# Kernel optimization log

Measured on AMD Instinct MI355X. Metric: run time of the kernel, lower is better.

The kernel has to match this reference:

```python
import jax, jax.numpy as jnp
import numpy as np

# Longformer-base-4096 dims; attention_window=128 -> one-sided window 64
B, S, D, H, L, F, V, NUM_LABELS = 1, 4096, 768, 12, 12, 3072, 50265, 100
DH = D // H
W = 64            # one-sided sliding window
NC = S // W       # number of query chunks
EPS = 1e-5
SCALE = float(1.0 / np.sqrt(DH))


def layer_norm(x, s, b):
    m = jnp.mean(x, axis=-1, keepdims=True)
    v = jnp.mean(jnp.square(x - m), axis=-1, keepdims=True)
    return (x - m) * jax.lax.rsqrt(v + EPS) * s + b


def heads(x):  # [B,S,D] -> [B,H,S,DH]
    return x.reshape(B, S, H, DH).transpose(0, 2, 1, 3)


def chunk3(t):  # [B,H,S,DH] -> [B,H,NC,3W,DH]: key blocks c-1,c,c+1 per query chunk c
    tp = jnp.pad(t, ((0, 0), (0, 0), (W, W), (0, 0)))
    tb = tp.reshape(B, H, NC + 2, W, DH)
    return jnp.concatenate([tb[:, :, i:i + NC] for i in range(3)], axis=3)


def _forward(input_ids, attention_mask, emb_tok, emb_pos, ln_emb_scale, ln_emb_bias,
             Wq, bq, Wk, bk, Wv, bv, Wqg, bqg, Wkg, bkg, Wvg, bvg, Wo, bo,
             ln1_scale, ln1_bias, Wf1, bf1, Wf2, bf2, ln2_scale, ln2_bias, Wc, bc):
    am = attention_mask > 0                      # [B,S]
    x = layer_norm(emb_tok[input_ids] + emb_pos[None, :, :], ln_emb_scale, ln_emb_bias)

    # static sliding-window masks, shared by all layers
    qi = jnp.arange(W)[:, None]
    kj = jnp.arange(3 * W)[None, :]
    band = (kj >= qi) & (kj <= qi + 2 * W)       # |key - query| <= W within a chunk triple
    kvalid = am & (jnp.arange(S)[None, :] > 0)   # global token (pos 0) excluded from window
    kp = jnp.pad(kvalid, ((0, 0), (W, W))).reshape(B, NC + 2, W)
    kmask = jnp.concatenate([kp[:, i:i + NC] for i in range(3)], axis=2)   # [B,NC,3W]
    win_mask = band[None, None, None] & kmask[:, None, :, None, :]         # [B,1,NC,W,3W]

    def layer(x, p):
        (wq, bq_, wk, bk_, wv, bv_, wqg, bqg_, wkg, bkg_, wvg, bvg_, wo, bo_,
         l1s, l1b, wf1, bf1_, wf2, bf2_, l2s, l2b) = p
        q = heads(x @ wq + bq_) * SCALE
        k = heads(x @ wk + bk_)
        v = heads(x @ wv + bv_)
        qc = q.reshape(B, H, NC, W, DH)
        k3, v3 = chunk3(k), chunk3(v)
        sc = jnp.einsum('bhcqd,bhckd->bhcqk', qc, k3)          # [B,H,NC,W,3W]
        sc = jnp.where(win_mask, sc, -1e9)
        # every token also attends to the global CLS key (standard K/V of pos 0)
        sg = jnp.einsum('bhsd,bhd->bhs', q, k[:, :, 0]).reshape(B, H, NC, W, 1)
        probs = jax.nn.softmax(jnp.concatenate([sg, sc], axis=-1), axis=-1)
        pg, pl = probs[..., 0], probs[..., 1:]
        ctx = jnp.einsum('bhcqk,bhckd->bhcqd', pl, v3).reshape(B, H, S, DH)
        ctx = ctx + pg.reshape(B, H, S, 1) * v[:, :, :1]
        # global token attends to everything with its own (global) projections
        qg = heads(x @ wqg + bqg_)[:, :, 0] * SCALE            # [B,H,DH]
        kg = heads(x @ wkg + bkg_)
        vg = heads(x @ wvg + bvg_)
        sgl = jnp.where(am[:, None, :], jnp.einsum('bhd,bhjd->bhj', qg, kg), -1e9)
        ctx0 = jnp.einsum('bhj,bhjd->bhd', jax.nn.softmax(sgl, axis=-1), vg)
        ctx = ctx.at[:, :, 0].set(ctx0)
        attn = ctx.transpose(0, 2, 1, 3).reshape(B, S, D) @ wo + bo_
        x1 = layer_norm(x + attn, l1s, l1b)
        h = jax.nn.gelu(x1 @ wf1 + bf1_, approximate=False)
        return layer_norm(x1 + h @ wf2 + bf2_, l2s, l2b), None

    params = (Wq, bq, Wk, bk, Wv, bv, Wqg, bqg, Wkg, bkg, Wvg, bvg, Wo, bo,
              ln1_scale, ln1_bias, Wf1, bf1, Wf2, bf2, ln2_scale, ln2_bias)
    x, _ = jax.lax.scan(layer, x, params)
    return x[:, 0] @ Wc + bc                                   # [B, NUM_LABELS]


def setup_inputs():
    key = jax.random.key(0)
    ks = jax.random.split(key, 40)
    it = iter(range(40))
    nrm = lambda shape: jax.random.normal(ks[next(it)], shape, dtype=jnp.float32) * 0.02
    z = lambda shape: jnp.zeros(shape, jnp.float32)
    o = lambda shape: jnp.ones(shape, jnp.float32)
    return {
        'input_ids': jax.random.randint(ks[next(it)], (B, S), 0, V, dtype=jnp.int32),
        'attention_mask': jnp.ones((B, S), dtype=jnp.int32),
        'emb_tok': nrm((V, D)), 'emb_pos': nrm((S, D)),
        'ln_emb_scale': o((D,)), 'ln_emb_bias': z((D,)),
        'Wq': nrm((L, D, D)), 'bq': z((L, D)),
        'Wk': nrm((L, D, D)), 'bk': z((L, D)),
        'Wv': nrm((L, D, D)), 'bv': z((L, D)),
        'Wqg': nrm((L, D, D)), 'bqg': z((L, D)),
        'Wkg': nrm((L, D, D)), 'bkg': z((L, D)),
        'Wvg': nrm((L, D, D)), 'bvg': z((L, D)),
        'Wo': nrm((L, D, D)), 'bo': z((L, D)),
        'ln1_scale': o((L, D)), 'ln1_bias': z((L, D)),
        'Wf1': nrm((L, D, F)), 'bf1': z((L, F)),
        'Wf2': nrm((L, F, D)), 'bf2': z((L, D)),
        'ln2_scale': o((L, D)), 'ln2_bias': z((L, D)),
        'Wc': nrm((D, NUM_LABELS)), 'bc': z((NUM_LABELS,)),
    }


def reference(input_ids, attention_mask, emb_tok, emb_pos, ln_emb_scale, ln_emb_bias,
              Wq, bq, Wk, bk, Wv, bv, Wqg, bqg, Wkg, bkg, Wvg, bvg, Wo, bo,
              ln1_scale, ln1_bias, Wf1, bf1, Wf2, bf2, ln2_scale, ln2_bias, Wc, bc):
    return _forward(input_ids, attention_mask, emb_tok, emb_pos, ln_emb_scale, ln_emb_bias,
                    Wq, bq, Wk, bk, Wv, bv, Wqg, bqg, Wkg, bkg, Wvg, bvg, Wo, bo,
                    ln1_scale, ln1_bias, Wf1, bf1, Wf2, bf2, ln2_scale, ln2_bias, Wc, bc)
```

## Files before the change

### kernel.cpp

```cpp
#include <hip/hip_runtime.h>
#include <hip/hip_bf16.h>

typedef unsigned short u16;
typedef __attribute__((ext_vector_type(8))) short bf16x8;
typedef __attribute__((ext_vector_type(4))) float f32x4;

constexpr int S = 4096, D = 768, H = 12, NL = 12, F = 3072, NLAB = 100, DH = 64;
constexpr int NQKV = 3840;
constexpr float SCALE = 0.125f;
constexpr float EPS = 1e-5f;

__device__ __forceinline__ float bits2f(u16 u) {
  union { unsigned int i; float f; } x; x.i = ((unsigned int)u) << 16; return x.f;
}
__device__ __forceinline__ u16 f2bbits(float f) {
  union { float f; unsigned int i; } x; x.f = f;
  return (u16)((x.i + 0x7FFFu + ((x.i >> 16) & 1u)) >> 16);
}
__device__ __forceinline__ float rdw(const void* p, size_t i, int isf32) {
  return isf32 ? ((const float*)p)[i] : bits2f(((const u16*)p)[i]);
}
__device__ __forceinline__ void gload16(const void* g, void* l) {
  __builtin_amdgcn_global_load_lds(
      (const __attribute__((address_space(1))) void*)g,
      (__attribute__((address_space(3))) void*)l, 16, 0, 0);
}

__global__ void detect_k(const void* lns, int* flag) {
  *flag = (*(const unsigned int*)lns == 0x3F800000u) ? 1 : 0;
}

struct PrepArgs {
  const void *Wq, *Wk, *Wv, *Wkg, *Wvg, *Wo, *Wqg, *Wf1, *Wf2;
  const void *bq, *bk, *bv, *bkg, *bvg, *bo, *bqg, *bf1, *bf2;
  size_t oDD, oDF, oD, oF;
  u16 *wt_qkv, *wt_o, *wt_qg, *wt_f1, *wt_f2;
  float* biasb;
  const int* flag;
};

__global__ __launch_bounds__(256) void prep_layer(PrepArgs a)
{
  const int b = blockIdx.x, t = threadIdx.x;
  const int isf32 = *a.flag;
  if (b < 8640) {
    __shared__ float tile[32][33];
    const void* src; size_t soff; int N, ld, rowoff, n0, k0;
    u16* dst; float scl = 1.f;
    if (b < 4032) {
      const int m = b / 576, ti = b - m * 576;
      soff = a.oDD; N = D; ld = D; rowoff = 0;
      switch (m) {
        case 0:  src = a.Wq;  dst = a.wt_qkv; scl = SCALE;  break;
        case 1:  src = a.Wk;  dst = a.wt_qkv; rowoff = 768; break;
        case 2:  src = a.Wv;  dst = a.wt_qkv; rowoff = 1536; break;
        case 3:  src = a.Wkg; dst = a.wt_qkv; rowoff = 2304; break;
        case 4:  src = a.Wvg; dst = a.wt_qkv; rowoff = 3072; break;
        case 5:  src = a.Wo;  dst = a.wt_o;   break;
        default: src = a.Wqg; dst = a.wt_qg;  scl = SCALE;  break;
      }
      n0 = (ti % 24) * 32; k0 = (ti / 24) * 32;
    } else if (b < 6336) {
      const int ti = b - 4032;
      src = a.Wf1; soff = a.oDF; N = F; dst = a.wt_f1; rowoff = 0; ld = D;
      n0 = (ti % 96) * 32; k0 = (ti / 96) * 32;
    } else {
      const int ti = b - 6336;
      src = a.Wf2; soff = a.oDF; N = D; dst = a.wt_f2; rowoff = 0; ld = F;
      n0 = (ti % 24) * 32; k0 = (ti / 24) * 32;
    }
    const int r = t >> 3, cc = (t & 7) << 2;
    const size_t si = soff + (size_t)(k0 + r) * N + n0 + cc;
    if (isf32) {
      const float4 v = *reinterpret_cast<const float4*>(&((const float*)src)[si]);
      tile[r][cc] = v.x * scl; tile[r][cc+1] = v.y * scl;
      tile[r][cc+2] = v.z * scl; tile[r][cc+3] = v.w * scl;
    } else {
      const ushort4 v = *reinterpret_cast<const ushort4*>(&((const u16*)src)[si]);
      tile[r][cc] = bits2f(v.x) * scl; tile[r][cc+1] = bits2f(v.y) * scl;
      tile[r][cc+2] = bits2f(v.z) * scl; tile[r][cc+3] = bits2f(v.w) * scl;
    }
    __syncthreads();
    const ushort4 ov = make_ushort4(f2bbits(tile[cc+0][r]), f2bbits(tile[cc+1][r]),
                                    f2bbits(tile[cc+2][r]), f2bbits(tile[cc+3][r]));
    *reinterpret_cast<ushort4*>(&dst[(size_t)(rowoff + n0 + r) * ld + k0 + cc]) = ov;
  } else {
    const int i = (b - 8640) * 256 + t;
    float v;
    if      (i < 768)  v = rdw(a.bq,  a.oD + i,        isf32) * SCALE;
    else if (i < 1536) v = rdw(a.bk,  a.oD + i - 768,  isf32);
    else if (i < 2304) v = rdw(a.bv,  a.oD + i - 1536, isf32);
    else if (i < 3072) v = rdw(a.bkg, a.oD + i - 2304, isf32);
    else if (i < 3840) v = rdw(a.bvg, a.oD + i - 3072, isf32);
    else if (i < 4608) v = rdw(a.bo,  a.oD + i - 3840, isf32);
    else if (i < 7680) v = rdw(a.bf1, a.oF + i - 4608, isf32);
    else if (i < 8448) v = rdw(a.bf2, a.oD + i - 7680, isf32);
    else               v = rdw(a.bqg, a.oD + i - 8448, isf32) * SCALE;
    a.biasb[i] = v;
  }
}

template<int BN>
__global__ __launch_bounds__(256) void mfma_gemm(
    const u16* __restrict__ A, const u16* __restrict__ BT,
    const float* __restrict__ bias,
    float* __restrict__ Cf, u16* __restrict__ Cb,
    int M, int N, int K, int act)
{
  constexpr int BM = 128, BK = 32;
  constexpr int WN = BN / 2;
  constexpr int NR = WN / 16;
  __shared__ u16 As[BM * BK];
  __shared__ u16 Bs[BN * BK];
  const int t = threadIdx.x;
  const int wid = t >> 6, lane = t & 63;
  const int wr = wid >> 1, wc = wid & 1;
  const int m0 = blockIdx.y * BM, n0 = blockIdx.x * BN;
  const int l_row = lane >> 2;
  const int l_kc = (lane & 3) << 3;

  f32x4 acc[4][NR];
#pragma unroll
  for (int m = 0; m < 4; ++m)
#pragma unroll
    for (int n = 0; n < NR; ++n)
      acc[m][n] = (f32x4){0.f, 0.f, 0.f, 0.f};

  const int frow = lane & 15;
  const int fkb = (lane >> 4) << 3;

  for (int kt = 0; kt < K; kt += BK) {
#pragma unroll
    for (int i = 0; i < 2; ++i) {
      const int ch = wid * 2 + i;
      gload16(&A[(size_t)(m0 + ch * 16 + l_row) * K + kt + l_kc], &As[ch * 512]);
    }
#pragma unroll
    for (int i = 0; i < BN / 64; ++i) {
      const int ch = wid * (BN / 64) + i;
      gload16(&BT[(size_t)(n0 + ch * 16 + l_row) * K + kt + l_kc], &Bs[ch * 512]);
    }
    __syncthreads();
    bf16x8 af[4], bfr[NR];
#pragma unroll
    for (int m = 0; m < 4; ++m)
      af[m] = *reinterpret_cast<const bf16x8*>(&As[(wr * 64 + m * 16 + frow) * BK + fkb]);
#pragma unroll
    for (int n = 0; n < NR; ++n)
      bfr[n] = *reinterpret_cast<const bf16x8*>(&Bs[(wc * WN + n * 16 + frow) * BK + fkb]);
#pragma unroll
    for (int m = 0; m < 4; ++m)
#pragma unroll
      for (int n = 0; n < NR; ++n)
        acc[m][n] = __builtin_amdgcn_mfma_f32_16x16x32_bf16(af[m], bfr[n], acc[m][n], 0, 0, 0);
    __syncthreads();
  }

  const int crow = (lane >> 4) << 2;
  const int ccol = lane & 15;
#pragma unroll
  for (int m = 0; m < 4; ++m) {
#pragma unroll
    for (int n = 0; n < NR; ++n) {
      const int gc = n0 + wc * WN + n * 16 + ccol;
      const float bv = bias[gc];
#pragma unroll
      for (int r = 0; r < 4; ++r) {
        const int gr = m0 + wr * 64 + m * 16 + crow + r;
        float x = acc[m][n][r] + bv;
        if (act) x = 0.5f * x * (1.0f + erff(x * 0.70710678118654752f));
        if (Cf) Cf[(size_t)gr * N + gc] = x;
        if (Cb) Cb[(size_t)gr * N + gc] = f2bbits(x);
      }
    }
  }
}

__global__ void embed_k(const int* __restrict__ ids, const void* __restrict__ tok,
                        const void* __restrict__ pos, float* __restrict__ out,
                        const int* __restrict__ flag)
{
  const int isf32 = *flag;
  const int s = blockIdx.x, t = threadIdx.x;
  const int id = ids[s];
  for (int c = t; c < D; c += 256)
    out[(size_t)s * D + c] = rdw(tok, (size_t)id * D + c, isf32) + rdw(pos, (size_t)s * D + c, isf32);
}

__global__ __launch_bounds__(256) void ln_res_k(
    const float* __restrict__ Ain, const float* __restrict__ Bin,
    const void* __restrict__ g, size_t goff, const void* __restrict__ b, size_t boff,
    float* __restrict__ Out, u16* __restrict__ Outb, const int* __restrict__ flag)
{
  __shared__ float buf[D];
  __shared__ float red[4];
  const int isf32 = *flag;
  const int r = blockIdx.x, t = threadIdx.x;
  float ls = 0.f;
  for (int c = t; c < D; c += 256) {
    float v = Ain[(size_t)r * D + c];
    if (Bin) v += Bin[(size_t)r * D + c];
    buf[c] = v; ls += v;
  }
#pragma unroll
  for (int off = 32; off; off >>= 1) ls += __shfl_xor(ls, off);
  if ((t & 63) == 0) red[t >> 6] = ls;
  __syncthreads();
  const float mean = (red[0] + red[1] + red[2] + red[3]) * (1.0f / D);
  __syncthreads();
  float lv = 0.f;
  for (int c = t; c < D; c += 256) { const float dd = buf[c] - mean; lv += dd * dd; }
#pragma unroll
  for (int off = 32; off; off >>= 1) lv += __shfl_xor(lv, off);
  if ((t & 63) == 0) red[t >> 6] = lv;
  __syncthreads();
  const float var = (red[0] + red[1] + red[2] + red[3]) * (1.0f / D);
  const float rstd = rsqrtf(var + EPS);
  for (int c = t; c < D; c += 256) {
    const float o = (buf[c] - mean) * rstd * rdw(g, goff + c, isf32) + rdw(b, boff + c, isf32);
    Out[(size_t)r * D + c] = o;
    if (Outb) Outb[(size_t)r * D + c] = f2bbits(o);
  }
}

__global__ __launch_bounds__(256) void qg_gemv(
    const u16* __restrict__ Xb, const u16* __restrict__ WgT,
    const float* __restrict__ biasb, float* __restrict__ QG)
{
  const int wid = threadIdx.x >> 6, lane = threadIdx.x & 63;
  const int o = blockIdx.x * 4 + wid;
  float a = 0.f;
#pragma unroll
  for (int j = 0; j < 12; ++j) {
    const int k = j * 64 + lane;
    a += bits2f(Xb[k]) * bits2f(WgT[(size_t)o * 768 + k]);
  }
#pragma unroll
  for (int off = 32; off; off >>= 1) a += __shfl_xor(a, off);
  if (lane == 0) QG[o] = a + biasb[8448 + o];
}

__global__ __launch_bounds__(256) void win_attn3(
    const u16* __restrict__ QKV, const int* __restrict__ am, u16* __restrict__ CTXb)
{
  __shared__ u16 Ql[64 * 64];
  __shared__ u16 Kl[224 * 64];
  __shared__ u16 Vt[64 * 232];
  __shared__ int kwin[224];
  const int c = blockIdx.x, h = blockIdx.y;
  const int t = threadIdx.x, w = t >> 6, lane = t & 63;
  const int base = c * 64 - 64, s0 = c * 64;

  for (int i = t; i < 1024; i += 256) {
    const int r = i >> 4, c4 = (i & 15) << 2;
    const ushort4 v = *reinterpret_cast<const ushort4*>(
        &QKV[(size_t)(s0 + r) * NQKV + h * 64 + c4]);
    *reinterpret_cast<ushort4*>((char*)Ql + ((r * 128 + c4 * 2) ^ ((r & 7) << 4))) = v;
  }
  for (int i = t; i < 3584; i += 256) {
    const int r = i >> 4, c4 = (i & 15) << 2;
    const int kp = (r < 192) ? (base + r) : ((r == 192) ? 0 : -1);
    ushort4 v = make_ushort4(0, 0, 0, 0);
    if (kp >= 0 && kp < S)
      v = *reinterpret_cast<const ushort4*>(&QKV[(size_t)kp * NQKV + 768 + h * 64 + c4]);
    *reinterpret_cast<ushort4*>((char*)Kl + ((r * 128 + c4 * 2) ^ ((r & 7) << 4))) = v;
  }
  for (int i = t; i < 3584; i += 256) {
    const int r = i >> 4, c4 = (i & 15) << 2;
    const int kp = (r < 192) ? (base + r) : ((r == 192) ? 0 : -1);
    ushort4 v = make_ushort4(0, 0, 0, 0);
    if (kp >= 0 && kp < S)
      v = *reinterpret_cast<const ushort4*>(&QKV[(size_t)kp * NQKV + 1536 + h * 64 + c4]);
    Vt[(c4 + 0) * 232 + r] = v.x;
    Vt[(c4 + 1) * 232 + r] = v.y;
    Vt[(c4 + 2) * 232 + r] = v.z;
    Vt[(c4 + 3) * 232 + r] = v.w;
  }
  if (t < 224) {
    const int kp = base + t;
    kwin[t] = (t < 192 && kp >= 1 && kp < S) ? am[kp] : 0;
  }
  __syncthreads();

  const int frow = lane & 15, fkb = (lane >> 4) << 3;
  const int crow = (lane >> 4) << 2, ccol = lane & 15;
  const int qrow = w * 16 + frow;

  bf16x8 aq[2];
#pragma unroll
  for (int ks = 0; ks < 2; ++ks)
    aq[ks] = *reinterpret_cast<const bf16x8*>(
        (const char*)Ql + ((qrow * 128 + (ks * 32 + fkb) * 2) ^ ((qrow & 7) << 4)));

  f32x4 sc[14];
#pragma unroll
  for (int tl = 0; tl < 14; ++tl) {
    sc[tl] = (f32x4){0.f, 0.f, 0.f, 0.f};
    const int key = tl * 16 + frow;
#pragma unroll
    for (int ks = 0; ks < 2; ++ks) {
      const bf16x8 bk = *reinterpret_cast<const bf16x8*>(
          (const char*)Kl + ((key * 128 + (ks * 32 + fkb) * 2) ^ ((key & 7) << 4)));
      sc[tl] = __builtin_amdgcn_mfma_f32_16x16x32_bf16(aq[ks], bk, sc[tl], 0, 0, 0);
    }
  }

  float m4[4] = {-1e30f, -1e30f, -1e30f, -1e30f};
#pragma unroll
  for (int tl = 0; tl < 14; ++tl) {
    const int kidx = tl * 16 + ccol;
    const int kw = kwin[kidx];
    const bool isg = (kidx == 192);
#pragma unroll
    for (int r = 0; r < 4; ++r) {
      const int qi = w * 16 + crow + r;
      const bool valid = isg || ((kidx >= qi) && (kidx <= qi + 128) && kw);
      const float v = valid ? sc[tl][r] : -1e30f;
      sc[tl][r] = v;
      m4[r] = fmaxf(m4[r], v);
    }
  }
#pragma unroll
  for (int r = 0; r < 4; ++r)
#pragma unroll
    for (int off = 8; off; off >>= 1) m4[r] = fmaxf(m4[r], __shfl_xor(m4[r], off));

  float ssum[4] = {0.f, 0.f, 0.f, 0.f};
#pragma unroll
  for (int tl = 0; tl < 14; ++tl)
#pragma unroll
    for (int r = 0; r < 4; ++r) {
      const float e = __expf(sc[tl][r] - m4[r]);
      sc[tl][r] = e;
      ssum[r] += e;
    }
#pragma unroll
  for (int r = 0; r < 4; ++r)
#pragma unroll
    for (int off = 8; off; off >>= 1) ssum[r] += __shfl_xor(ssum[r], off);

  __syncthreads();
  u16* Pl = Kl;
#pragma unroll
  for (int tl = 0; tl < 14; ++tl) {
    const int kidx = tl * 16 + ccol;
#pragma unroll
    for (int r = 0; r < 4; ++r) {
      const int row = crow + r;
      *(u16*)((char*)Pl + w * 7168 + ((row * 448 + kidx * 2) ^ ((row & 7) << 4))) =
          f2bbits(sc[tl][r]);
    }
  }
  __syncthreads();

  bf16x8 pa[7];
#pragma unroll
  for (int ks = 0; ks < 7; ++ks)
    pa[ks] = *reinterpret_cast<const bf16x8*>(
        (const char*)Pl + w * 7168 + ((frow * 448 + (ks * 32 + fkb) * 2) ^ ((frow & 7) << 4)));

  f32x4 av[4];
#pragma unroll
  for (int n = 0; n < 4; ++n) {
    av[n] = (f32x4){0.f, 0.f, 0.f, 0.f};
#pragma unroll
    for (int ks = 0; ks < 7; ++ks) {
      const bf16x8 bv = *reinterpret_cast<const bf16x8*>(&Vt[(n * 16 + frow) * 232 + ks * 32 + fkb]);
      av[n] = __builtin_amdgcn_mfma_f32_16x16x32_bf16(pa[ks], bv, av[n], 0, 0, 0);
    }
  }
  float inv[4];
#pragma unroll
  for (int r = 0; r < 4; ++r) inv[r] = 1.f / ssum[r];
#pragma unroll
  for (int n = 0; n < 4; ++n)
#pragma unroll
    for (int r = 0; r < 4; ++r) {
      const int s = s0 + w * 16 + crow + r;
      CTXb[(size_t)s * D + h * 64 + n * 16 + ccol] = f2bbits(av[n][r] * inv[r]);
    }
}

__global__ __launch_bounds__(256) void glob_part(
    const u16* __restrict__ QKV, const float* __restrict__ QG,
    const int* __restrict__ am, float* __restrict__ gp)
{
  __shared__ float qsh[DH];
  __shared__ float se[256];
  __shared__ float red[4];
  __shared__ float part[4][DH];
  const int seg = blockIdx.x, h = blockIdx.y, t = threadIdx.x;
  const int j0 = seg * 256;
  if (t < DH) qsh[t] = QG[h * DH + t];
  __syncthreads();
  const int j = j0 + t;
  float a = 0.f;
  const u16* kr = &QKV[(size_t)j * NQKV + 2304 + h * 64];
  for (int d = 0; d < 64; ++d) a += qsh[d] * bits2f(kr[d]);
  a = (am[j] > 0) ? a : -1e9f;
  float m = a;
#pragma unroll
  for (int off = 32; off; off >>= 1) m = fmaxf(m, __shfl_xor(m, off));
  if ((t & 63) == 0) red[t >> 6] = m;
  __syncthreads();
  m = fmaxf(fmaxf(red[0], red[1]), fmaxf(red[2], red[3]));
  const float e = __expf(a - m);
  se[t] = e;
  float ls = e;
#pragma unroll
  for (int off = 32; off; off >>= 1) ls += __shfl_xor(ls, off);
  __syncthreads();
  if ((t & 63) == 0) red[t >> 6] = ls;
  __syncthreads();
  const float lsum = red[0] + red[1] + red[2] + red[3];
  const int g = t >> 6, d = t & 63;
  float acc = 0.f;
  for (int jj = g; jj < 256; jj += 4)
    acc += se[jj] * bits2f(QKV[(size_t)(j0 + jj) * NQKV + 3072 + h * 64 + d]);
  part[g][d] = acc;
  __syncthreads();
  if (t < 64) {
    float* o = &gp[(size_t)(h * 16 + seg) * 66];
    o[t] = part[0][t] + part[1][t] + part[2][t] + part[3][t];
    if (t == 0) { o[64] = m; o[65] = lsum; }
  }
}

__global__ void glob_comb(const float* __restrict__ gp, u16* __restrict__ CTXb)
{
  const int h = blockIdx.x, t = threadIdx.x;
  float M = -1e30f;
  for (int i = 0; i < 16; ++i) M = fmaxf(M, gp[(size_t)(h * 16 + i) * 66 + 64]);
  float L = 0.f, acc = 0.f;
  for (int i = 0; i < 16; ++i) {
    const float* o = &gp[(size_t)(h * 16 + i) * 66];
    const float w = __expf(o[64] - M);
    L += o[65] * w;
    acc += o[t] * w;
  }
  CTXb[h * 64 + t] = f2bbits(acc / L);
}

__global__ void cls_k(const float* __restrict__ X, const void* __restrict__ Wc,
                      const void* __restrict__ bc, void* __restrict__ out,
                      const int* __restrict__ flag)
{
  const int isf32 = *flag;
  const int n = threadIdx.x;
  if (n >= NLAB) return;
  float a = rdw(bc, n, isf32);
  for (int d = 0; d < D; ++d) a += X[d] * rdw(Wc, (size_t)d * NLAB + n, isf32);
  if (isf32) ((float*)out)[n] = a;
  else ((u16*)out)[n] = f2bbits(a);
}

extern "C" void kernel_launch(void* const* d_in, const int* in_sizes, int n_in,
                              void* d_out, int out_size, void* d_ws, size_t ws_size,
                              hipStream_t stream)
{
  const int*  ids = (const int*)d_in[0];
  const int*  am  = (const int*)d_in[1];
  const void* emb_tok = d_in[2];
  const void* emb_pos = d_in[3];
  const void* ln_e_g  = d_in[4];
  const void* ln_e_b  = d_in[5];
  const void* Wq  = d_in[6];  const void* bq  = d_in[7];
  const void* Wk  = d_in[8];  const void* bk  = d_in[9];
  const void* Wv  = d_in[10]; const void* bv  = d_in[11];
  const void* Wqg = d_in[12]; const void* bqg = d_in[13];
  const void* Wkg = d_in[14]; const void* bkg = d_in[15];
  const void* Wvg = d_in[16]; const void* bvg = d_in[17];
  const void* Wo  = d_in[18]; const void* bo  = d_in[19];
  const void* l1g = d_in[20]; const void* l1b = d_in[21];
  const void* Wf1 = d_in[22]; const void* bf1 = d_in[23];
  const void* Wf2 = d_in[24]; const void* bf2 = d_in[25];
  const void* l2g = d_in[26]; const void* l2b = d_in[27];
  const void* Wc  = d_in[28]; const void* bc  = d_in[29];

  float* ws = (float*)d_ws;
  const size_t SD = (size_t)S * D;
  size_t cur = 0;
  auto af32 = [&](size_t n) { float* p = ws + cur; cur += n; return p; };
  auto au16 = [&](size_t n_u16) { u16* p = (u16*)(ws + cur); cur += n_u16 / 2; return p; };

  float* X     = af32(SD);
  float* X1    = af32(SD);
  float* TMP   = af32(SD);
  u16*   QKV16 = au16(5 * SD);
  u16*   Hb    = au16((size_t)S * F);
  u16*   Xb    = au16(SD);
  u16*   X1b   = au16(SD);
  u16*   CTXb  = au16(SD);
  u16*   wt_qkv = au16((size_t)NQKV * D);
  u16*   wt_o   = au16((size_t)D * D);
  u16*   wt_qg  = au16((size_t)D * D);
  u16*   wt_f1  = au16((size_t)F * D);
  u16*   wt_f2  = au16((size_t)D * F);
  float* biasb  = af32(9216);
  float* QGb    = af32(768);
  float* gp     = af32((size_t)H * 16 * 66);
  int*   flag   = (int*)af32(4);

  detect_k<<<1, 1, 0, stream>>>(ln_e_g, flag);
  embed_k<<<S, 256, 0, stream>>>(ids, emb_tok, emb_pos, TMP, flag);
  ln_res_k<<<S, 256, 0, stream>>>(TMP, nullptr, ln_e_g, 0, ln_e_b, 0, X, Xb, flag);

  for (int l = 0; l < NL; ++l) {
    PrepArgs pa;
    pa.Wq = Wq; pa.Wk = Wk; pa.Wv = Wv; pa.Wkg = Wkg; pa.Wvg = Wvg;
    pa.Wo = Wo; pa.Wqg = Wqg; pa.Wf1 = Wf1; pa.Wf2 = Wf2;
    pa.bq = bq; pa.bk = bk; pa.bv = bv; pa.bkg = bkg; pa.bvg = bvg;
    pa.bo = bo; pa.bqg = bqg; pa.bf1 = bf1; pa.bf2 = bf2;
    pa.oDD = (size_t)l * D * D; pa.oDF = (size_t)l * D * F;
    pa.oD = (size_t)l * D; pa.oF = (size_t)l * F;
    pa.wt_qkv = wt_qkv; pa.wt_o = wt_o; pa.wt_qg = wt_qg;
    pa.wt_f1 = wt_f1; pa.wt_f2 = wt_f2; pa.biasb = biasb; pa.flag = flag;
    prep_layer<<<8676, 256, 0, stream>>>(pa);

    mfma_gemm<128><<<dim3(NQKV / 128, S / 128), 256, 0, stream>>>(
        Xb, wt_qkv, biasb, nullptr, QKV16, S, NQKV, D, 0);
    qg_gemv<<<192, 256, 0, stream>>>(Xb, wt_qg, biasb, QGb);
    win_attn3<<<dim3(S / 64, H), 256, 0, stream>>>(QKV16, am, CTXb);
    glob_part<<<dim3(16, H), 256, 0, stream>>>(QKV16, QGb, am, gp);
    glob_comb<<<H, 64, 0, stream>>>(gp, CTXb);
    mfma_gemm<64><<<dim3(D / 64, S / 128), 256, 0, stream>>>(
        CTXb, wt_o, biasb + 3840, TMP, nullptr, S, D, D, 0);
    ln_res_k<<<S, 256, 0, stream>>>(X, TMP, l1g, pa.oD, l1b, pa.oD, X1, X1b, flag);
    mfma_gemm<128><<<dim3(F / 128, S / 128), 256, 0, stream>>>(
        X1b, wt_f1, biasb + 4608, nullptr, Hb, S, F, D, 1);
    mfma_gemm<64><<<dim3(D / 64, S / 128), 256, 0, stream>>>(
        Hb, wt_f2, biasb + 7680, TMP, nullptr, S, D, F, 0);
    ln_res_k<<<S, 256, 0, stream>>>(X1, TMP, l2g, pa.oD, l2b, pa.oD, X, Xb, flag);
  }
  cls_k<<<1, 128, 0, stream>>>(X, Wc, bc, d_out, flag);
}
```

Before: 3.369 ms.

## Split-K the narrow output GEMMs and reduce partials in the LayerNorm kernel

The Wo and FFN2 GEMMs (N=768) launch only 192 blocks, so they are split along K into 2 and 4 slices that write fp32 partial sums to separate buffers. The residual LayerNorm kernel now adds up to four partial buffers, which fuses the split-K reduction into it. The global-attention key dot product is also vectorised with 16-byte loads, and the classifier head is parallelised across waves with shuffle reductions. The cost is extra fp32 partial traffic (up to 4x SD writes and reads) and a larger workspace.

```diff
diff --git a/kernel.cpp b/kernel.cpp
--- a/kernel.cpp
+++ b/kernel.cpp
@@ -100,7 +100,7 @@
   }
 }
 
-template<int BN>
+template<int BN, int SPLITK>
 __global__ __launch_bounds__(256) void mfma_gemm(
     const u16* __restrict__ A, const u16* __restrict__ BT,
     const float* __restrict__ bias,
@@ -116,6 +116,9 @@
   const int wid = t >> 6, lane = t & 63;
   const int wr = wid >> 1, wc = wid & 1;
   const int m0 = blockIdx.y * BM, n0 = blockIdx.x * BN;
+  const int z = (SPLITK > 1) ? blockIdx.z : 0;
+  const int kLen = K / SPLITK;
+  const int k0 = z * kLen;
   const int l_row = lane >> 2;
   const int l_kc = (lane & 3) << 3;
 
@@ -129,7 +132,7 @@
   const int frow = lane & 15;
   const int fkb = (lane >> 4) << 3;
 
-  for (int kt = 0; kt < K; kt += BK) {
+  for (int kt = k0; kt < k0 + kLen; kt += BK) {
 #pragma unroll
     for (int i = 0; i < 2; ++i) {
       const int ch = wid * 2 + i;
@@ -156,6 +159,7 @@
     __syncthreads();
   }
 
+  float* Cp = (SPLITK > 1) ? (Cf + (size_t)z * M * N) : Cf;
   const int crow = (lane >> 4) << 2;
   const int ccol = lane & 15;
 #pragma unroll
@@ -163,14 +167,14 @@
 #pragma unroll
     for (int n = 0; n < NR; ++n) {
       const int gc = n0 + wc * WN + n * 16 + ccol;
-      const float bv = bias[gc];
+      const float bv = (z == 0) ? bias[gc] : 0.f;
 #pragma unroll
       for (int r = 0; r < 4; ++r) {
         const int gr = m0 + wr * 64 + m * 16 + crow + r;
         float x = acc[m][n][r] + bv;
-        if (act) x = 0.5f * x * (1.0f + erff(x * 0.70710678118654752f));
-        if (Cf) Cf[(size_t)gr * N + gc] = x;
-        if (Cb) Cb[(size_t)gr * N + gc] = f2bbits(x);
+        if (SPLITK == 1 && act) x = 0.5f * x * (1.0f + erff(x * 0.70710678118654752f));
+        if (Cp) Cp[(size_t)gr * N + gc] = x;
+        if (SPLITK == 1 && Cb) Cb[(size_t)gr * N + gc] = f2bbits(x);
       }
     }
   }
@@ -188,7 +192,9 @@
 }
 
 __global__ __launch_bounds__(256) void ln_res_k(
-    const float* __restrict__ Ain, const float* __restrict__ Bin,
+    const float* __restrict__ Ain,
+    const float* __restrict__ P0, const float* __restrict__ P1,
+    const float* __restrict__ P2, const float* __restrict__ P3,
     const void* __restrict__ g, size_t goff, const void* __restrict__ b, size_t boff,
     float* __restrict__ Out, u16* __restrict__ Outb, const int* __restrict__ flag)
 {
@@ -198,8 +204,12 @@
   const int r = blockIdx.x, t = threadIdx.x;
   float ls = 0.f;
   for (int c = t; c < D; c += 256) {
-    float v = Ain[(size_t)r * D + c];
-    if (Bin) v += Bin[(size_t)r * D + c];
+    const size_t i = (size_t)r * D + c;
+    float v = Ain[i];
+    if (P0) v += P0[i];
+    if (P1) v += P1[i];
+    if (P2) v += P2[i];
+    if (P3) v += P3[i];
     buf[c] = v; ls += v;
   }
 #pragma unroll
@@ -396,7 +406,13 @@
   const int j = j0 + t;
   float a = 0.f;
   const u16* kr = &QKV[(size_t)j * NQKV + 2304 + h * 64];
-  for (int d = 0; d < 64; ++d) a += qsh[d] * bits2f(kr[d]);
+#pragma unroll
+  for (int v8 = 0; v8 < 8; ++v8) {
+    const bf16x8 kv = *reinterpret_cast<const bf16x8*>(&kr[v8 * 8]);
+#pragma unroll
+    for (int e = 0; e < 8; ++e)
+      a += qsh[v8 * 8 + e] * bits2f((u16)kv[e]);
+  }
   a = (am[j] > 0) ? a : -1e9f;
   float m = a;
 #pragma unroll
@@ -441,17 +457,28 @@
   CTXb[h * 64 + t] = f2bbits(acc / L);
 }
 
-__global__ void cls_k(const float* __restrict__ X, const void* __restrict__ Wc,
-                      const void* __restrict__ bc, void* __restrict__ out,
-                      const int* __restrict__ flag)
+__global__ __launch_bounds__(256) void cls_k(
+    const float* __restrict__ X, const void* __restrict__ Wc,
+    const void* __restrict__ bc, void* __restrict__ out,
+    const int* __restrict__ flag)
 {
   const int isf32 = *flag;
-  const int n = threadIdx.x;
+  const int wid = threadIdx.x >> 6, lane = threadIdx.x & 63;
+  const int n = blockIdx.x * 4 + wid;
   if (n >= NLAB) return;
-  float a = rdw(bc, n, isf32);
-  for (int d = 0; d < D; ++d) a += X[d] * rdw(Wc, (size_t)d * NLAB + n, isf32);
-  if (isf32) ((float*)out)[n] = a;
-  else ((u16*)out)[n] = f2bbits(a);
+  float a = 0.f;
+#pragma unroll
+  for (int j = 0; j < 12; ++j) {
+    const int k = j * 64 + lane;
+    a += X[k] * rdw(Wc, (size_t)k * NLAB + n, isf32);
+  }
+#pragma unroll
+  for (int off = 32; off; off >>= 1) a += __shfl_xor(a, off);
+  if (lane == 0) {
+    a += rdw(bc, n, isf32);
+    if (isf32) ((float*)out)[n] = a;
+    else ((u16*)out)[n] = f2bbits(a);
+  }
 }
 
 extern "C" void kernel_launch(void* const* d_in, const int* in_sizes, int n_in,
@@ -485,7 +512,7 @@
 
   float* X     = af32(SD);
   float* X1    = af32(SD);
-  float* TMP   = af32(SD);
+  float* TMP   = af32(4 * SD);
   u16*   QKV16 = au16(5 * SD);
   u16*   Hb    = au16((size_t)S * F);
   u16*   Xb    = au16(SD);
@@ -501,9 +528,15 @@
   float* gp     = af32((size_t)H * 16 * 66);
   int*   flag   = (int*)af32(4);
 
+  float* T0 = TMP;
+  float* T1 = TMP + SD;
+  float* T2 = TMP + 2 * SD;
+  float* T3 = TMP + 3 * SD;
+
   detect_k<<<1, 1, 0, stream>>>(ln_e_g, flag);
-  embed_k<<<S, 256, 0, stream>>>(ids, emb_tok, emb_pos, TMP, flag);
-  ln_res_k<<<S, 256, 0, stream>>>(TMP, nullptr, ln_e_g, 0, ln_e_b, 0, X, Xb, flag);
+  embed_k<<<S, 256, 0, stream>>>(ids, emb_tok, emb_pos, T0, flag);
+  ln_res_k<<<S, 256, 0, stream>>>(T0, nullptr, nullptr, nullptr, nullptr,
+                                  ln_e_g, 0, ln_e_b, 0, X, Xb, flag);
 
   for (int l = 0; l < NL; ++l) {
     PrepArgs pa;
@@ -517,20 +550,22 @@
     pa.wt_f1 = wt_f1; pa.wt_f2 = wt_f2; pa.biasb = biasb; pa.flag = flag;
     prep_layer<<<8676, 256, 0, stream>>>(pa);
 
-    mfma_gemm<128><<<dim3(NQKV / 128, S / 128), 256, 0, stream>>>(
+    mfma_gemm<128, 1><<<dim3(NQKV / 128, S / 128), 256, 0, stream>>>(
         Xb, wt_qkv, biasb, nullptr, QKV16, S, NQKV, D, 0);
     qg_gemv<<<192, 256, 0, stream>>>(Xb, wt_qg, biasb, QGb);
     win_attn3<<<dim3(S / 64, H), 256, 0, stream>>>(QKV16, am, CTXb);
     glob_part<<<dim3(16, H), 256, 0, stream>>>(QKV16, QGb, am, gp);
     glob_comb<<<H, 64, 0, stream>>>(gp, CTXb);
-    mfma_gemm<64><<<dim3(D / 64, S / 128), 256, 0, stream>>>(
+    mfma_gemm<64, 2><<<dim3(D / 64, S / 128, 2), 256, 0, stream>>>(
         CTXb, wt_o, biasb + 3840, TMP, nullptr, S, D, D, 0);
-    ln_res_k<<<S, 256, 0, stream>>>(X, TMP, l1g, pa.oD, l1b, pa.oD, X1, X1b, flag);
-    mfma_gemm<128><<<dim3(F / 128, S / 128), 256, 0, stream>>>(
+    ln_res_k<<<S, 256, 0, stream>>>(X, T0, T1, nullptr, nullptr,
+                                    l1g, pa.oD, l1b, pa.oD, X1, X1b, flag);
+    mfma_gemm<128, 1><<<dim3(F / 128, S / 128), 256, 0, stream>>>(
         X1b, wt_f1, biasb + 4608, nullptr, Hb, S, F, D, 1);
-    mfma_gemm<64><<<dim3(D / 64, S / 128), 256, 0, stream>>>(
+    mfma_gemm<64, 4><<<dim3(D / 64, S / 128, 4), 256, 0, stream>>>(
         Hb, wt_f2, biasb + 7680, TMP, nullptr, S, D, F, 0);
-    ln_res_k<<<S, 256, 0, stream>>>(X1, TMP, l2g, pa.oD, l2b, pa.oD, X, Xb, flag);
-  }
-  cls_k<<<1, 128, 0, stream>>>(X, Wc, bc, d_out, flag);
-}
+    ln_res_k<<<S, 256, 0, stream>>>(X1, T0, T1, T2, T3,
+                                    l2g, pa.oD, l2b, pa.oD, X, Xb, flag);
+  }
+  cls_k<<<25, 256, 0, stream>>>(X, Wc, bc, d_out, flag);
+}
```

Measured after the change: 3.182 ms. -5.6%, faster.
